# Optimization experiments

Measured on AMD Instinct MI355X. Metric: run time of the kernel, lower is better.

Reference implementation:

```python
import jax, jax.numpy as jnp
import numpy as np

B, S, D_IN, HID = 64, 512, 1024, 4096  # HID = 4 * state_size
HS = HID // 4


def setup_inputs() -> dict:
    key = jax.random.key(0)
    k1, k2, k3 = jax.random.split(key, 3)
    x = jax.random.normal(k1, (B, S, D_IN), dtype=jnp.float32)
    wx = jax.random.uniform(k2, (HID, D_IN), minval=-0.1, maxval=0.1, dtype=jnp.float32)
    wh = jax.random.uniform(k3, (HID, HS), minval=-0.1, maxval=0.1, dtype=jnp.float32)
    bx = jnp.zeros((HID,), dtype=jnp.float32)
    bh = jnp.zeros((HID,), dtype=jnp.float32)
    return {"x": x, "wx": wx, "wh": wh, "bx": bx, "bh": bh}


def _lstm(x, wx, wh, bx, bh):
    batch = x.shape[0]
    hs = wh.shape[1]
    # Precompute the input contribution for all timesteps in one big GEMM.
    # xg: [S, B, HID]
    xg = jnp.einsum('bsd,gd->sbg', x, wx) + bx + bh

    def step(carry, xg_t):
        h, c = carry
        gates = xg_t + h @ wh.T  # [B, HID]
        i, f, g, o = jnp.split(gates, 4, axis=1)
        i = jax.nn.sigmoid(i)
        f = jax.nn.sigmoid(f)
        g = jnp.tanh(g)
        o = jax.nn.sigmoid(o)
        c = f * c + i * g
        h = o * jnp.tanh(c)
        return (h, c), h

    h0 = jnp.zeros((batch, hs), dtype=x.dtype)
    c0 = jnp.zeros((batch, hs), dtype=x.dtype)
    (h, c), hs_seq = jax.lax.scan(step, (h0, c0), xg)
    out = jnp.transpose(hs_seq, (1, 0, 2))  # [B, S, HS]
    return out, (h, c)


def reference(x, wx, wh, bx, bh):
    return _lstm(x, wx, wh, bx, bh)
```

## Files before the change

kernel.cpp:

```cpp
#include <hip/hip_runtime.h>
#include <hip/hip_bf16.h>
#include <stdint.h>


typedef __attribute__((ext_vector_type(8))) short short8;
typedef __attribute__((ext_vector_type(4))) float floatx4;

#define S_LEN 512
#define BATCH 64
#define DIN   1024
#define HID   4096
#define HS    1024

#define XG2_OFF   0ull
#define XBF_OFF   268435456ull
#define WXBF_OFF  335544320ull
#define WHBF_OFF  343932928ull
#define HBUF_OFF  352321536ull
#define FLAG_OFF  XBF_OFF

__device__ __forceinline__ unsigned short f2bf(float f) {
  unsigned int u = __float_as_uint(f);
  u += 0x7fffu + ((u >> 16) & 1u);
  return (unsigned short)(u >> 16);
}
__device__ __forceinline__ float bf2f(unsigned short s) {
  return __uint_as_float(((unsigned int)s) << 16);
}

__device__ __forceinline__ void async_ld16(const void* g, const void* l) {
  __builtin_amdgcn_global_load_lds(
      (const __attribute__((address_space(1))) unsigned int*)g,
      (__attribute__((address_space(3))) unsigned int*)l,
      16, 0, 0);
}

__device__ __forceinline__ short8 load16_llc(const void* p) {
  floatx4 r;
  asm volatile("global_load_dwordx4 %0, %1, off sc0 sc1"
               : "=v"(r) : "v"(p) : "memory");
  return __builtin_bit_cast(short8, r);
}
__device__ __forceinline__ void store2_llc(void* p, unsigned int v) {
  asm volatile("global_store_short %0, %1, off sc0 sc1"
               :: "v"(p), "v"(v) : "memory");
}
__device__ __forceinline__ void st4_llc(void* p, unsigned int v) {
  asm volatile("global_store_dword %0, %1, off sc0 sc1"
               :: "v"(p), "v"(v) : "memory");
}
__device__ __forceinline__ int ld_flag_llc(const int* p) {
  int v;
  asm volatile("global_load_dword %0, %1, off sc0 sc1\n\t"
               "s_waitcnt vmcnt(0)"
               : "=v"(v) : "v"(p) : "memory");
  return v;
}

__device__ __forceinline__ float sigmoidf_(float x) {
  return 1.0f / (1.0f + __expf(-x));
}
__device__ __forceinline__ float tanhf_(float x) {
  return 2.0f / (1.0f + __expf(-2.0f * x)) - 1.0f;
}

__global__ void cvt_kernel(const float* __restrict__ src,
                           unsigned short* __restrict__ dst, int n4) {
  int i = blockIdx.x * blockDim.x + threadIdx.x;
  if (i < n4) {
    float4 v = ((const float4*)src)[i];
    ushort4 o;
    o.x = f2bf(v.x); o.y = f2bf(v.y); o.z = f2bf(v.z); o.w = f2bf(v.w);
    ((ushort4*)dst)[i] = o;
  }
}

__global__ void zero_kernel(unsigned int* __restrict__ p, int n) {
  int i = blockIdx.x * blockDim.x + threadIdx.x;
  if (i < n) p[i] = 0u;
}

__global__ __launch_bounds__(256) void pregemm_kernel(
    const unsigned short* __restrict__ A,
    const unsigned short* __restrict__ Bw,
    const float* __restrict__ bx, const float* __restrict__ bh,
    unsigned short* __restrict__ xg2) {
  __shared__ unsigned short As[128 * 32];
  __shared__ unsigned short Bs[128 * 32];
  const int tid = threadIdx.x;
  const int lane = tid & 63, wv = tid >> 6;
  const int l15 = lane & 15, lq = lane >> 4;
  const int m0 = blockIdx.y * 128, n0 = blockIdx.x * 128;
  const int wm = (wv >> 1) * 64, wn = (wv & 1) * 64;

  floatx4 acc[4][4];
#pragma unroll
  for (int i = 0; i < 4; i++)
#pragma unroll
    for (int j = 0; j < 4; j++) acc[i][j] = (floatx4){0.f, 0.f, 0.f, 0.f};

  for (int k0 = 0; k0 < DIN; k0 += 32) {
#pragma unroll
    for (int q = 0; q < 2; q++) {
      const int e = (q * 256 + tid) * 8;
      const int r = e >> 5, c = e & 31;
      async_ld16(A + (size_t)(m0 + r) * DIN + k0 + c, (unsigned short*)As + e);
      async_ld16(Bw + (size_t)(n0 + r) * DIN + k0 + c, (unsigned short*)Bs + e);
    }
    __syncthreads();
    short8 af[4], bfv[4];
#pragma unroll
    for (int i = 0; i < 4; i++)
      af[i] = *(const short8*)&As[(wm + i * 16 + l15) * 32 + lq * 8];
#pragma unroll
    for (int j = 0; j < 4; j++)
      bfv[j] = *(const short8*)&Bs[(wn + j * 16 + l15) * 32 + lq * 8];
#pragma unroll
    for (int i = 0; i < 4; i++)
#pragma unroll
      for (int j = 0; j < 4; j++)
        acc[i][j] = __builtin_amdgcn_mfma_f32_16x16x32_bf16(af[i], bfv[j],
                                                            acc[i][j], 0, 0, 0);
    __syncthreads();
  }

#pragma unroll
  for (int j = 0; j < 4; j++) {
    const int col = n0 + wn + j * 16 + l15;
    const float bias = bx[col] + bh[col];
    const int gate = col >> 10;
    const int c1 = col & 1023;
    const int wslice = c1 >> 4, cc = c1 & 15;
    const int n_idx = gate * 16 + cc;
#pragma unroll
    for (int i = 0; i < 4; i++) {
#pragma unroll
      for (int r = 0; r < 4; r++) {
        const int m = m0 + wm + i * 16 + lq * 4 + r;
        const int b = m >> 9, t = m & 511;
        const size_t idx =
            ((size_t)(t * 256 + ((b >> 4) * 64 + wslice)) * 16 + (b & 15)) * 64 +
            n_idx;
        xg2[idx] = f2bf(acc[i][j][r] + bias);
      }
    }
  }
}

__global__ __launch_bounds__(256, 1) void lstm_kernel(
    const unsigned short* __restrict__ whbf,
    const unsigned short* __restrict__ xg2,
    unsigned short* __restrict__ hbuf,
    int* __restrict__ flags,
    float* __restrict__ out,
    float* __restrict__ outh, float* __restrict__ outc) {
  __shared__ float gpart[4 * 16 * 68];

  const int tid = threadIdx.x;
  const int lane = tid & 63, kq = tid >> 6;
  const int l15 = lane & 15, lq = lane >> 4;
  const int wg = blockIdx.x;
  const int group = wg >> 6, wslice = wg & 63;
  const int j0 = wslice * 16;

  short8 bfrag[4][8];
#pragma unroll
  for (int j = 0; j < 4; j++) {
    const size_t grow = (size_t)(j * 1024 + j0 + l15) * HS;
#pragma unroll
    for (int kc = 0; kc < 8; kc++)
      bfrag[j][kc] = *(const short8*)&whbf[grow + kq * 256 + kc * 32 + lq * 8];
  }

  const int eb = tid >> 4;
  const int ec = tid & 15;
  const int gb = group * 16 + eb;
  float c_state = 0.0f;

  const size_t arow = (size_t)(group * 16 + l15) * HS + kq * 256 + lq * 8;
  const int* fp = flags +
      ((size_t)((group * 64 + kq * 16 + (lane >> 2)) * 4 + (lane & 3))) * 16;

  const unsigned short* xr0 = xg2 + ((size_t)(0 * 256 + wg) * 16 + eb) * 64 + ec;
  unsigned short xv0 = xr0[0], xv1 = xr0[16], xv2 = xr0[32], xv3 = xr0[48];

  for (int t = 0; t < S_LEN; t++) {
    if (t > 0) {
      while (true) {
        int v = ld_flag_llc(fp);
        if (__all(v >= t)) break;
        __builtin_amdgcn_s_sleep(1);
      }
    }

    const unsigned short* hp = hbuf + (size_t)(t & 1) * (BATCH * HS) + arow;
    short8 a[8];
#pragma unroll
    for (int kc = 0; kc < 8; kc++) a[kc] = load16_llc(&hp[kc * 32]);
    asm volatile("s_waitcnt vmcnt(0)"
                 : "+v"(a[0]), "+v"(a[1]), "+v"(a[2]), "+v"(a[3]),
                   "+v"(a[4]), "+v"(a[5]), "+v"(a[6]), "+v"(a[7])
                 :: "memory");

    floatx4 acc0 = (floatx4){0.f, 0.f, 0.f, 0.f};
    floatx4 acc1 = acc0, acc2 = acc0, acc3 = acc0;
#pragma unroll
    for (int kc = 0; kc < 8; kc++) {
      acc0 = __builtin_amdgcn_mfma_f32_16x16x32_bf16(a[kc], bfrag[0][kc], acc0, 0, 0, 0);
      acc1 = __builtin_amdgcn_mfma_f32_16x16x32_bf16(a[kc], bfrag[1][kc], acc1, 0, 0, 0);
      acc2 = __builtin_amdgcn_mfma_f32_16x16x32_bf16(a[kc], bfrag[2][kc], acc2, 0, 0, 0);
      acc3 = __builtin_amdgcn_mfma_f32_16x16x32_bf16(a[kc], bfrag[3][kc], acc3, 0, 0, 0);
    }
#pragma unroll
    for (int r = 0; r < 4; r++) {
      const int row = (kq * 16 + lq * 4 + r) * 68;
      gpart[row + 0 * 16 + l15] = acc0[r];
      gpart[row + 1 * 16 + l15] = acc1[r];
      gpart[row + 2 * 16 + l15] = acc2[r];
      gpart[row + 3 * 16 + l15] = acc3[r];
    }
    __syncthreads();

    float g0 = bf2f(xv0), g1 = bf2f(xv1), g2 = bf2f(xv2), g3 = bf2f(xv3);
#pragma unroll
    for (int q = 0; q < 4; q++) {
      const float* gp = &gpart[(q * 16 + eb) * 68 + ec];
      g0 += gp[0]; g1 += gp[16]; g2 += gp[32]; g3 += gp[48];
    }
    const float i_ = sigmoidf_(g0);
    const float f_ = sigmoidf_(g1);
    const float gg = tanhf_(g2);
    const float o_ = sigmoidf_(g3);
    c_state = f_ * c_state + i_ * gg;
    const float h = o_ * tanhf_(c_state);

    store2_llc(&hbuf[(size_t)((t + 1) & 1) * (BATCH * HS) + (size_t)gb * HS +
                     j0 + ec],
               (unsigned int)f2bf(h));

    if (t == S_LEN - 1) {
      out[((size_t)gb * S_LEN + t) * HS + j0 + ec] = h;
      outh[gb * HS + j0 + ec] = h;
      outc[gb * HS + j0 + ec] = c_state;
      break;
    }

    asm volatile("s_waitcnt vmcnt(0)" ::: "memory");
    if (lane == 0)
      st4_llc(&flags[(wg * 4 + kq) * 16], (unsigned int)(t + 1));

    const unsigned short* xb =
        xg2 + ((size_t)((t + 1) * 256 + wg) * 16 + eb) * 64 + ec;
    unsigned short nx0 = xb[0], nx1 = xb[16], nx2 = xb[32], nx3 = xb[48];

    __builtin_nontemporal_store(h, &out[((size_t)gb * S_LEN + t) * HS + j0 + ec]);

    __syncthreads();

    xv0 = nx0; xv1 = nx1; xv2 = nx2; xv3 = nx3;
  }
}

extern "C" void kernel_launch(void* const* d_in, const int* in_sizes, int n_in,
                              void* d_out, int out_size, void* d_ws,
                              size_t ws_size, hipStream_t stream) {
  const float* x  = (const float*)d_in[0];
  const float* wx = (const float*)d_in[1];
  const float* wh = (const float*)d_in[2];
  const float* bx = (const float*)d_in[3];
  const float* bh = (const float*)d_in[4];
  char* ws = (char*)d_ws;
  unsigned short* xg2  = (unsigned short*)(ws + XG2_OFF);
  unsigned short* xbf  = (unsigned short*)(ws + XBF_OFF);
  unsigned short* wxbf = (unsigned short*)(ws + WXBF_OFF);
  unsigned short* whbf = (unsigned short*)(ws + WHBF_OFF);
  unsigned short* hbuf = (unsigned short*)(ws + HBUF_OFF);
  int* flags = (int*)(ws + FLAG_OFF);

  float* out  = (float*)d_out;
  float* outh = out + (size_t)BATCH * S_LEN * HS;
  float* outc = outh + BATCH * HS;

  cvt_kernel<<<(33554432 / 4) / 256, 256, 0, stream>>>(x, xbf, 33554432 / 4);
  cvt_kernel<<<(4194304 / 4) / 256, 256, 0, stream>>>(wx, wxbf, 4194304 / 4);
  cvt_kernel<<<(4194304 / 4) / 256, 256, 0, stream>>>(wh, whbf, 4194304 / 4);
  zero_kernel<<<256, 256, 0, stream>>>((unsigned int*)(ws + HBUF_OFF), 65536);

  dim3 pg(HID / 128, (BATCH * S_LEN) / 128);
  pregemm_kernel<<<pg, 256, 0, stream>>>(xbf, wxbf, bx, bh, xg2);

  zero_kernel<<<64, 256, 0, stream>>>((unsigned int*)flags, 16384);

  lstm_kernel<<<256, 256, 0, stream>>>(whbf, xg2, hbuf, flags, out, outh, outc);
}
```

Before: 2.130 ms.

## Use 64 larger LSTM workgroups with LDS-staged hidden state and fewer flags

The recurrent kernel now runs as 64 workgroups of 1024 threads instead of 256 of 256. Each workgroup covers 64 hidden columns for a 16-row batch group. The previous hidden state is loaded cooperatively into LDS once per step and shared by all 16 waves, rather than each wave reading it from global memory. Flag polling now involves 16 producer waves per group instead of 64, the t=0 matmul is skipped so the hbuf zeroing launch can be removed, and one barrier per step is dropped. The costs are more LDS per block, an extra barrier around the staging, and only 64 blocks, so much of the GPU sits idle.

```diff
diff --git a/kernel.cpp b/kernel.cpp
--- a/kernel.cpp
+++ b/kernel.cpp
@@ -147,21 +147,23 @@
   }
 }
 
-__global__ __launch_bounds__(256, 1) void lstm_kernel(
+__global__ __launch_bounds__(1024, 1) void lstm_kernel(
     const unsigned short* __restrict__ whbf,
     const unsigned short* __restrict__ xg2,
     unsigned short* __restrict__ hbuf,
     int* __restrict__ flags,
     float* __restrict__ out,
     float* __restrict__ outh, float* __restrict__ outc) {
-  __shared__ float gpart[4 * 16 * 68];
+  __shared__ unsigned short hstage[16 * 1032];
+  __shared__ float gpart[4 * 16 * 260];
 
   const int tid = threadIdx.x;
-  const int lane = tid & 63, kq = tid >> 6;
+  const int lane = tid & 63, wv = tid >> 6;
   const int l15 = lane & 15, lq = lane >> 4;
   const int wg = blockIdx.x;
-  const int group = wg >> 6, wslice = wg & 63;
-  const int j0 = wslice * 16;
+  const int group = wg >> 4, wslice = wg & 15;
+  const int kq = wv & 3, jq = wv >> 2;
+  const int j0 = wslice * 64 + jq * 16;
 
   short8 bfrag[4][8];
 #pragma unroll
@@ -172,17 +174,21 @@
       bfrag[j][kc] = *(const short8*)&whbf[grow + kq * 256 + kc * 32 + lq * 8];
   }
 
-  const int eb = tid >> 4;
-  const int ec = tid & 15;
+  const int eb = tid >> 6;
+  const int ec = tid & 63;
   const int gb = group * 16 + eb;
   float c_state = 0.0f;
 
-  const size_t arow = (size_t)(group * 16 + l15) * HS + kq * 256 + lq * 8;
-  const int* fp = flags +
-      ((size_t)((group * 64 + kq * 16 + (lane >> 2)) * 4 + (lane & 3))) * 16;
-
-  const unsigned short* xr0 = xg2 + ((size_t)(0 * 256 + wg) * 16 + eb) * 64 + ec;
-  unsigned short xv0 = xr0[0], xv1 = xr0[16], xv2 = xr0[32], xv3 = xr0[48];
+  const int srow = lane >> 3;
+  const int scol = wv * 64 + (lane & 7) * 8;
+
+  const int* fp = flags + ((size_t)((group * 16 + wv) * 16 + (lane & 15))) * 4;
+  int* myflag = flags + ((size_t)(wg * 16 + wv)) * 4;
+
+  const int owg = group * 64 + wslice * 4 + (ec >> 4);
+  const size_t xgb0 = ((size_t)(0 * 256 + owg) * 16 + eb) * 64 + (ec & 15);
+  unsigned short xv0 = xg2[xgb0], xv1 = xg2[xgb0 + 16], xv2 = xg2[xgb0 + 32],
+                 xv3 = xg2[xgb0 + 48];
 
   for (int t = 0; t < S_LEN; t++) {
     if (t > 0) {
@@ -191,41 +197,50 @@
         if (__all(v >= t)) break;
         __builtin_amdgcn_s_sleep(1);
       }
-    }
-
-    const unsigned short* hp = hbuf + (size_t)(t & 1) * (BATCH * HS) + arow;
-    short8 a[8];
-#pragma unroll
-    for (int kc = 0; kc < 8; kc++) a[kc] = load16_llc(&hp[kc * 32]);
-    asm volatile("s_waitcnt vmcnt(0)"
-                 : "+v"(a[0]), "+v"(a[1]), "+v"(a[2]), "+v"(a[3]),
-                   "+v"(a[4]), "+v"(a[5]), "+v"(a[6]), "+v"(a[7])
-                 :: "memory");
-
-    floatx4 acc0 = (floatx4){0.f, 0.f, 0.f, 0.f};
-    floatx4 acc1 = acc0, acc2 = acc0, acc3 = acc0;
-#pragma unroll
-    for (int kc = 0; kc < 8; kc++) {
-      acc0 = __builtin_amdgcn_mfma_f32_16x16x32_bf16(a[kc], bfrag[0][kc], acc0, 0, 0, 0);
-      acc1 = __builtin_amdgcn_mfma_f32_16x16x32_bf16(a[kc], bfrag[1][kc], acc1, 0, 0, 0);
-      acc2 = __builtin_amdgcn_mfma_f32_16x16x32_bf16(a[kc], bfrag[2][kc], acc2, 0, 0, 0);
-      acc3 = __builtin_amdgcn_mfma_f32_16x16x32_bf16(a[kc], bfrag[3][kc], acc3, 0, 0, 0);
-    }
-#pragma unroll
-    for (int r = 0; r < 4; r++) {
-      const int row = (kq * 16 + lq * 4 + r) * 68;
-      gpart[row + 0 * 16 + l15] = acc0[r];
-      gpart[row + 1 * 16 + l15] = acc1[r];
-      gpart[row + 2 * 16 + l15] = acc2[r];
-      gpart[row + 3 * 16 + l15] = acc3[r];
+      const unsigned short* hp = hbuf + (size_t)(t & 1) * (BATCH * HS);
+      const size_t gr = (size_t)(group * 16 + srow) * HS + scol;
+      short8 s0 = load16_llc(&hp[gr]);
+      short8 s1 = load16_llc(&hp[gr + 8 * HS]);
+      asm volatile("s_waitcnt vmcnt(0)"
+                   : "+v"(s0), "+v"(s1) :: "memory");
+      *(short8*)&hstage[srow * 1032 + scol] = s0;
+      *(short8*)&hstage[(srow + 8) * 1032 + scol] = s1;
     }
     __syncthreads();
 
+    if (t > 0) {
+      short8 a[8];
+#pragma unroll
+      for (int kc = 0; kc < 8; kc++)
+        a[kc] = *(const short8*)&hstage[l15 * 1032 + kq * 256 + kc * 32 +
+                                        lq * 8];
+      floatx4 acc0 = (floatx4){0.f, 0.f, 0.f, 0.f};
+      floatx4 acc1 = acc0, acc2 = acc0, acc3 = acc0;
+#pragma unroll
+      for (int kc = 0; kc < 8; kc++) {
+        acc0 = __builtin_amdgcn_mfma_f32_16x16x32_bf16(a[kc], bfrag[0][kc], acc0, 0, 0, 0);
+        acc1 = __builtin_amdgcn_mfma_f32_16x16x32_bf16(a[kc], bfrag[1][kc], acc1, 0, 0, 0);
+        acc2 = __builtin_amdgcn_mfma_f32_16x16x32_bf16(a[kc], bfrag[2][kc], acc2, 0, 0, 0);
+        acc3 = __builtin_amdgcn_mfma_f32_16x16x32_bf16(a[kc], bfrag[3][kc], acc3, 0, 0, 0);
+      }
+#pragma unroll
+      for (int r = 0; r < 4; r++) {
+        const int row = (kq * 16 + lq * 4 + r) * 260;
+        gpart[row + 0 * 64 + jq * 16 + l15] = acc0[r];
+        gpart[row + 1 * 64 + jq * 16 + l15] = acc1[r];
+        gpart[row + 2 * 64 + jq * 16 + l15] = acc2[r];
+        gpart[row + 3 * 64 + jq * 16 + l15] = acc3[r];
+      }
+    }
+    __syncthreads();
+
     float g0 = bf2f(xv0), g1 = bf2f(xv1), g2 = bf2f(xv2), g3 = bf2f(xv3);
-#pragma unroll
-    for (int q = 0; q < 4; q++) {
-      const float* gp = &gpart[(q * 16 + eb) * 68 + ec];
-      g0 += gp[0]; g1 += gp[16]; g2 += gp[32]; g3 += gp[48];
+    if (t > 0) {
+#pragma unroll
+      for (int q = 0; q < 4; q++) {
+        const float* gp = &gpart[(q * 16 + eb) * 260 + ec];
+        g0 += gp[0]; g1 += gp[64]; g2 += gp[128]; g3 += gp[192];
+      }
     }
     const float i_ = sigmoidf_(g0);
     const float f_ = sigmoidf_(g1);
@@ -235,27 +250,26 @@
     const float h = o_ * tanhf_(c_state);
 
     store2_llc(&hbuf[(size_t)((t + 1) & 1) * (BATCH * HS) + (size_t)gb * HS +
-                     j0 + ec],
+                     wslice * 64 + ec],
                (unsigned int)f2bf(h));
 
     if (t == S_LEN - 1) {
-      out[((size_t)gb * S_LEN + t) * HS + j0 + ec] = h;
-      outh[gb * HS + j0 + ec] = h;
-      outc[gb * HS + j0 + ec] = c_state;
+      out[((size_t)gb * S_LEN + t) * HS + wslice * 64 + ec] = h;
+      outh[(size_t)gb * HS + wslice * 64 + ec] = h;
+      outc[(size_t)gb * HS + wslice * 64 + ec] = c_state;
       break;
     }
 
     asm volatile("s_waitcnt vmcnt(0)" ::: "memory");
-    if (lane == 0)
-      st4_llc(&flags[(wg * 4 + kq) * 16], (unsigned int)(t + 1));
-
-    const unsigned short* xb =
-        xg2 + ((size_t)((t + 1) * 256 + wg) * 16 + eb) * 64 + ec;
-    unsigned short nx0 = xb[0], nx1 = xb[16], nx2 = xb[32], nx3 = xb[48];
-
-    __builtin_nontemporal_store(h, &out[((size_t)gb * S_LEN + t) * HS + j0 + ec]);
-
-    __syncthreads();
+    if (lane == 0) st4_llc(myflag, (unsigned int)(t + 1));
+
+    const size_t xgb =
+        ((size_t)((t + 1) * 256 + owg) * 16 + eb) * 64 + (ec & 15);
+    unsigned short nx0 = xg2[xgb], nx1 = xg2[xgb + 16], nx2 = xg2[xgb + 32],
+                   nx3 = xg2[xgb + 48];
+
+    __builtin_nontemporal_store(
+        h, &out[((size_t)gb * S_LEN + t) * HS + wslice * 64 + ec]);
 
     xv0 = nx0; xv1 = nx1; xv2 = nx2; xv3 = nx3;
   }
@@ -284,12 +298,11 @@
   cvt_kernel<<<(33554432 / 4) / 256, 256, 0, stream>>>(x, xbf, 33554432 / 4);
   cvt_kernel<<<(4194304 / 4) / 256, 256, 0, stream>>>(wx, wxbf, 4194304 / 4);
   cvt_kernel<<<(4194304 / 4) / 256, 256, 0, stream>>>(wh, whbf, 4194304 / 4);
-  zero_kernel<<<256, 256, 0, stream>>>((unsigned int*)(ws + HBUF_OFF), 65536);
 
   dim3 pg(HID / 128, (BATCH * S_LEN) / 128);
   pregemm_kernel<<<pg, 256, 0, stream>>>(xbf, wxbf, bx, bh, xg2);
 
-  zero_kernel<<<64, 256, 0, stream>>>((unsigned int*)flags, 16384);
-
-  lstm_kernel<<<256, 256, 0, stream>>>(whbf, xg2, hbuf, flags, out, outh, outc);
-}
+  zero_kernel<<<16, 256, 0, stream>>>((unsigned int*)flags, 4096);
+
+  lstm_kernel<<<64, 1024, 0, stream>>>(whbf, xg2, hbuf, flags, out, outh, outc);
+}
```

After: 5.096 ms. 2.39x slower.
